# Kernel tuning notes

Measured on AMD Instinct MI355X. Metric: run time of the kernel, lower is better.

The kernel has to match this reference:

```python
import jax, jax.numpy as jnp
import numpy as np

B, NJ, NM = 64, 30, 20
N = NJ * NM          # 600 operation nodes per FJSP instance
IN_DIM, H = 2, 128


def _bn(h):
    # torch BatchNorm1d in training mode, gamma=1/beta=0 (module init), stats over all nodes
    m = h.mean(axis=(0, 1))
    v = h.var(axis=(0, 1))
    return (h - m) / jnp.sqrt(v + 1e-5)


def setup_inputs() -> dict:
    key = jax.random.key(0)
    ks = jax.random.split(key, 20)
    x = jax.random.normal(ks[0], (B, N, IN_DIM), jnp.float32)
    graph_pool = jnp.full((B, N), 1.0 / N, jnp.float32)   # average graph pooling weights
    padded_nei = jnp.zeros((1,), jnp.int32)               # unused (sum pooling path)
    adj = (jax.random.uniform(ks[1], (B, N, N)) < 0.01).astype(jnp.float32)
    adj = jnp.minimum(adj + jnp.eye(N, dtype=jnp.float32)[None], 1.0)  # self-loops
    candidate = jax.random.randint(ks[2], (B, NJ), 0, N)
    a_index = jax.random.randint(ks[3], (B,), 0, NJ)
    mask = jax.random.uniform(ks[4], (B, NJ)) < 0.2
    mask = mask.at[jnp.arange(B), a_index].set(False)     # chosen action never masked
    mask_mch = jax.random.uniform(ks[5], (B, N, NM)) < 0.3
    dur = jax.random.uniform(ks[6], (B, N, NM), dtype=jnp.float32)
    old_action = jax.random.randint(ks[7], (B,), 0, N)
    mch_pool = jax.random.normal(ks[8], (B, H), jnp.float32)

    def w(k, i, o):
        return jax.random.normal(k, (i, o), jnp.float32) * (1.0 / np.sqrt(i))

    z = lambda n: jnp.zeros((n,), jnp.float32)            # biases init to 0 in module
    return dict(
        x=x, graph_pool=graph_pool, padded_nei=padded_nei, adj=adj,
        candidate=candidate, mask=mask, mask_mch=mask_mch, dur=dur,
        a_index=a_index, old_action=old_action, mch_pool=mch_pool,
        W1_0=w(ks[9], IN_DIM, H), b1_0=z(H), W2_0=w(ks[10], H, H), b2_0=z(H),
        W1_1=w(ks[11], H, H), b1_1=z(H), W2_1=w(ks[12], H, H), b2_1=z(H),
        Wa1=w(ks[13], 3 * H, H), ba1=z(H), Wa2=w(ks[14], H, H), ba2=z(H),
        Wa3=w(ks[15], H, 1), ba3=z(1),
        Wc1=w(ks[16], H, H), bc1=z(H), Wc2=w(ks[17], H, 1), bc2=z(1),
    )


def reference(x, graph_pool, padded_nei, adj, candidate, mask, mask_mch, dur,
              a_index, old_action, mch_pool,
              W1_0, b1_0, W2_0, b2_0, W1_1, b1_1, W2_1, b2_1,
              Wa1, ba1, Wa2, ba2, Wa3, ba3, Wc1, bc1, Wc2, bc2):
    # --- GIN encoder: num_layers-1 = 2 message-passing layers, sum pooling ---
    h = x
    for (W1, b1, W2, b2) in ((W1_0, b1_0, W2_0, b2_0), (W1_1, b1_1, W2_1, b2_1)):
        pooled = jnp.einsum('bnm,bmd->bnd', adj, h)         # neighbor sum (adj has self-loops)
        h1 = jax.nn.relu(_bn(pooled @ W1 + b1))             # MLP hidden (BN inside MLP)
        h = jax.nn.relu(_bn(h1 @ W2 + b2))                  # layer BN + relu
    h_nodes = h                                             # [B, N, H]
    h_pooled = jnp.einsum('bn,bnd->bd', graph_pool, h_nodes)  # [B, H]

    # --- gather candidate features, concat pooled contexts ---
    cand_feat = jnp.take_along_axis(h_nodes, candidate[:, :, None], axis=1)  # [B, NJ, H]
    concat = jnp.concatenate([
        cand_feat,
        jnp.broadcast_to(h_pooled[:, None, :], cand_feat.shape),
        jnp.broadcast_to(mch_pool[:, None, :], cand_feat.shape)], axis=-1)   # [B, NJ, 3H]

    # --- MLPActor(3 layers, tanh) ---
    a = jnp.tanh(concat @ Wa1 + ba1)
    a = jnp.tanh(a @ Wa2 + ba2)
    scores = (a @ Wa3 + ba3).squeeze(-1) * 10.0             # [B, NJ]
    scores = jnp.where(mask, -jnp.inf, scores)
    logpi = jax.nn.log_softmax(scores, axis=1)
    pi = jnp.exp(logpi)
    log_a = jnp.take_along_axis(logpi, a_index[:, None], axis=1)[:, 0]
    entropy = -jnp.sum(jnp.where(pi > 0, pi * logpi, 0.0), axis=1)

    # --- gather action-dependent tensors (detached in torch) ---
    b_idx = jnp.arange(B)
    action_node = dur[b_idx, old_action]                    # [B, NM]
    action_feature = h_nodes[b_idx, old_action]             # [B, H]
    mask_mch_action = mask_mch[b_idx, old_action][:, None, :]  # [B, 1, NM]

    # --- MLPCritic(2 layers, tanh) ---
    v = jnp.tanh(h_pooled @ Wc1 + bc1) @ Wc2 + bc2          # [B, 1]

    sg = jax.lax.stop_gradient
    return (entropy, v, log_a, sg(action_node), sg(action_feature),
            mask_mch_action, sg(h_pooled))
```

## Files before the change

### kernel.cpp

```cpp
#include <hip/hip_runtime.h>
#include <hip/hip_bf16.h>

#define BB 64
#define NJ 30
#define NM 20
#define NN 600
#define HH 128
#define NROWS (BB*NN)
#define CAP 48

typedef __attribute__((ext_vector_type(8))) short short8;
typedef __attribute__((ext_vector_type(4))) float f32x4;

#define STATS_B   0
#define FLAGS_B   36864
#define ZERO_B    36880
#define WTB_B     37120
#define NBRCNT_B  143104
#define NBRIDX_B  296704
#define POOLED0_B 7669504
#define T1_B      7976704
#define P1_B      27637504

#define OUT_ENT   0
#define OUT_V     64
#define OUT_LOGA  128
#define OUT_ANODE 192
#define OUT_AFEAT 1472
#define OUT_MMCH  9664
#define OUT_HPOOL 10944

__device__ __forceinline__ bool mask_at(const void* p, int layout, long i) {
    if (layout == 2) return ((const float*)p)[i] != 0.f;
    if (layout == 1) return ((const unsigned char*)p)[i] != 0;
    return ((const int*)p)[i] != 0;
}

__device__ __forceinline__ short bf16rne(float f) {
    unsigned u = __float_as_uint(f);
    return (short)((u + 0x7fffu + ((u >> 16) & 1u)) >> 16);
}
__device__ __forceinline__ float bf2f(unsigned h) {
    return __uint_as_float(h << 16);
}
__device__ __forceinline__ unsigned packbf(float a, float b) {
    return ((unsigned)(unsigned short)bf16rne(a)) |
           (((unsigned)(unsigned short)bf16rne(b)) << 16);
}

__global__ __launch_bounds__(256) void k_sparse(const float* __restrict__ adj,
                                                const float* __restrict__ x,
                                                int* __restrict__ nbr_cnt,
                                                int* __restrict__ nbr_idx,
                                                float* __restrict__ pooled0,
                                                const void* mask_p, const void* maskmch_p,
                                                int* flags,
                                                const float* __restrict__ Wa,
                                                const float* __restrict__ Wb,
                                                const float* __restrict__ Wc,
                                                unsigned short* __restrict__ wT) {
    int bid = blockIdx.x;
    int tid = threadIdx.x;
    if (bid < 289) {
        if (bid >= 97) {
            int bid2 = bid - 97;
            int mat = bid2 >> 6;
            int idx = ((bid2 & 63) << 8) + tid;
            const float* W = mat == 0 ? Wa : (mat == 1 ? Wb : Wc);
            int k = idx >> 7, c = idx & 127;
            wT[mat * 16384 + c * HH + k] = (unsigned short)bf16rne(W[idx]);
        } else {
            unsigned agg = 0;
            int which;
            if (bid == 0) {
                which = 0;
                const unsigned* p = (const unsigned*)mask_p;
                unsigned w0 = (tid < 480) ? p[tid] : 0u;
                unsigned w1 = (tid + 256 < 480) ? p[tid + 256] : 0u;
                agg = w0 | w1;
            } else {
                which = 1;
                const unsigned* p = (const unsigned*)maskmch_p + (size_t)(bid - 1) * 200;
                agg = (tid < 200) ? p[tid] : 0u;
            }
            int f = 0;
            if (((agg >> 24) & 0xffu) == 0x3fu) f |= 1;
            if ((((agg >> 8) & 0xffu) == 1u) || (((agg >> 16) & 0xffu) == 1u) ||
                (((agg >> 24) & 0xffu) == 1u)) f |= 2;
#pragma unroll
            for (int off = 1; off < 64; off <<= 1) f |= __shfl_xor(f, off);
            if ((tid & 63) == 0 && f) atomicOr(&flags[which], f);
        }
    }

    int wrow = bid * 4 + (tid >> 6);
    int lane = tid & 63;
    int b = wrow / NN;
    const float4* arow = (const float4*)(adj + (size_t)wrow * NN);
    int* irow = nbr_idx + (size_t)wrow * CAP;
    const float* xb = x + (size_t)b * NN * 2;
    float4 vv[3];
    vv[0] = arow[lane];
    vv[1] = arow[64 + lane];
    vv[2] = (128 + lane < 150) ? arow[128 + lane] : make_float4(0.f, 0.f, 0.f, 0.f);
    int cnt = 0;
    float p0 = 0.f, p1 = 0.f;
#pragma unroll
    for (int it = 0; it < 3; ++it) {
        float4 v = vv[it];
        int col0 = it * 256 + lane * 4;
        bool m0 = v.x != 0.f, m1 = v.y != 0.f, m2 = v.z != 0.f, m3 = v.w != 0.f;
        int c_lane = (int)m0 + (int)m1 + (int)m2 + (int)m3;
        int inc = c_lane;
#pragma unroll
        for (int off = 1; off < 64; off <<= 1) {
            int t = __shfl_up(inc, off);
            if (lane >= off) inc += t;
        }
        int pos = cnt + inc - c_lane;
        if (m0) {
            if (pos < CAP) irow[pos] = col0;
            float2 xv = *(const float2*)&xb[col0 * 2];
            p0 += xv.x; p1 += xv.y; ++pos;
        }
        if (m1) {
            if (pos < CAP) irow[pos] = col0 + 1;
            float2 xv = *(const float2*)&xb[(col0 + 1) * 2];
            p0 += xv.x; p1 += xv.y; ++pos;
        }
        if (m2) {
            if (pos < CAP) irow[pos] = col0 + 2;
            float2 xv = *(const float2*)&xb[(col0 + 2) * 2];
            p0 += xv.x; p1 += xv.y; ++pos;
        }
        if (m3) {
            if (pos < CAP) irow[pos] = col0 + 3;
            float2 xv = *(const float2*)&xb[(col0 + 3) * 2];
            p0 += xv.x; p1 += xv.y; ++pos;
        }
        cnt += __shfl(inc, 63);
    }
#pragma unroll
    for (int off = 1; off < 64; off <<= 1) {
        p0 += __shfl_xor(p0, off);
        p1 += __shfl_xor(p1, off);
    }
    if (lane == 0) {
        nbr_cnt[wrow] = cnt < CAP ? cnt : CAP;
        pooled0[(size_t)wrow * 2]     = p0;
        pooled0[(size_t)wrow * 2 + 1] = p1;
    }
}

__global__ __launch_bounds__(256) void k_p0stats(const float* __restrict__ pooled0,
                                                 float* __restrict__ out5) {
    __shared__ float red[4][5];
    int i = blockIdx.x * 256 + threadIdx.x;
    float p0 = pooled0[(size_t)i * 2], p1 = pooled0[(size_t)i * 2 + 1];
    float v[5] = {p0, p1, p0 * p0, p1 * p1, p0 * p1};
#pragma unroll
    for (int j = 0; j < 5; ++j)
#pragma unroll
        for (int off = 1; off < 64; off <<= 1) v[j] += __shfl_xor(v[j], off);
    int lane = threadIdx.x & 63, w = threadIdx.x >> 6;
    if (lane == 0)
#pragma unroll
        for (int j = 0; j < 5; ++j) red[w][j] = v[j];
    __syncthreads();
    if (threadIdx.x == 0)
#pragma unroll
        for (int j = 0; j < 5; ++j)
            atomicAdd(&out5[j], red[0][j] + red[1][j] + red[2][j] + red[3][j]);
}

template<int MODE>
__global__ __launch_bounds__(256) void k_stage(const void* __restrict__ t_in_v,
                                               const float* __restrict__ pooled0,
                                               const float* __restrict__ W1,
                                               const unsigned short* __restrict__ wT,
                                               const float* __restrict__ stats_in,
                                               unsigned short* __restrict__ t_out,
                                               float* __restrict__ stats_out) {
    __shared__ float sm_mean[HH], sm_inv[HH];
    __shared__ float smS[4][32], smQ[4][32];
    int tid = threadIdx.x;
    if (MODE == 0 && tid < HH) {
        float S0 = stats_in[0], S1 = stats_in[1], Q0 = stats_in[2], Q1 = stats_in[3], P01 = stats_in[4];
        float w0 = W1[tid], w1 = W1[HH + tid];
        float m = (S0 * w0 + S1 * w1) * (1.f / NROWS);
        float eq = (Q0 * w0 * w0 + Q1 * w1 * w1 + 2.f * P01 * w0 * w1) * (1.f / NROWS);
        sm_mean[tid] = m;
        sm_inv[tid] = 1.f / sqrtf(eq - m * m + 1e-5f);
    }
    if (MODE == 1 && tid < HH) {
        float s = stats_in[tid], q = stats_in[HH + tid];
        float m = s * (1.f / NROWS);
        sm_mean[tid] = m;
        sm_inv[tid] = 1.f / sqrtf(q * (1.f / NROWS) - m * m + 1e-5f);
    }
    __syncthreads();

    const unsigned short* tin = (const unsigned short*)t_in_v;
    int lane = tid & 63, wave = tid >> 6;
    int r16 = lane & 15, kg = lane >> 4;
    int rowbase = (blockIdx.x >> 2) * 64 + wave * 16;
    int colq = blockIdx.x & 3;

    f32x4 acc[2];
#pragma unroll
    for (int t = 0; t < 2; ++t)
#pragma unroll
        for (int i = 0; i < 4; ++i) acc[t][i] = 0.f;

    float p0 = 0.f, p1 = 0.f;
    if (MODE == 0) {
        p0 = pooled0[(size_t)(rowbase + r16) * 2];
        p1 = pooled0[(size_t)(rowbase + r16) * 2 + 1];
    }

#pragma unroll
    for (int ks = 0; ks < 4; ++ks) {
        int kb = ks * 32 + kg * 8;
        short8 afr;
        {
            float av[8];
            if (MODE == 0) {
                float4 wa0 = *(const float4*)&W1[kb];
                float4 wa1 = *(const float4*)&W1[kb + 4];
                float4 wb0 = *(const float4*)&W1[HH + kb];
                float4 wb1 = *(const float4*)&W1[HH + kb + 4];
                av[0] = p0 * wa0.x + p1 * wb0.x; av[1] = p0 * wa0.y + p1 * wb0.y;
                av[2] = p0 * wa0.z + p1 * wb0.z; av[3] = p0 * wa0.w + p1 * wb0.w;
                av[4] = p0 * wa1.x + p1 * wb1.x; av[5] = p0 * wa1.y + p1 * wb1.y;
                av[6] = p0 * wa1.z + p1 * wb1.z; av[7] = p0 * wa1.w + p1 * wb1.w;
            } else {
                short8 raw = *(const short8*)&tin[(size_t)(rowbase + r16) * HH + kb];
#pragma unroll
                for (int j = 0; j < 8; ++j) av[j] = bf2f((unsigned short)raw[j]);
            }
            float4 m0 = *(const float4*)&sm_mean[kb];
            float4 m1 = *(const float4*)&sm_mean[kb + 4];
            float4 i0 = *(const float4*)&sm_inv[kb];
            float4 i1 = *(const float4*)&sm_inv[kb + 4];
            av[0] = fmaxf((av[0] - m0.x) * i0.x, 0.f);
            av[1] = fmaxf((av[1] - m0.y) * i0.y, 0.f);
            av[2] = fmaxf((av[2] - m0.z) * i0.z, 0.f);
            av[3] = fmaxf((av[3] - m0.w) * i0.w, 0.f);
            av[4] = fmaxf((av[4] - m1.x) * i1.x, 0.f);
            av[5] = fmaxf((av[5] - m1.y) * i1.y, 0.f);
            av[6] = fmaxf((av[6] - m1.z) * i1.z, 0.f);
            av[7] = fmaxf((av[7] - m1.w) * i1.w, 0.f);
#pragma unroll
            for (int j = 0; j < 8; ++j) afr[j] = bf16rne(av[j]);
        }
#pragma unroll
        for (int t = 0; t < 2; ++t) {
            short8 bfr = *(const short8*)&wT[(size_t)((colq * 2 + t) * 16 + r16) * HH + kb];
            acc[t] = __builtin_amdgcn_mfma_f32_16x16x32_bf16(afr, bfr, acc[t], 0, 0, 0);
        }
    }

#pragma unroll
    for (int t = 0; t < 2; ++t) {
        int lc = t * 16 + r16;
        int col = colq * 32 + lc;
        float s = 0.f, q = 0.f;
#pragma unroll
        for (int i = 0; i < 4; ++i) {
            float v = acc[t][i];
            t_out[(size_t)(rowbase + kg * 4 + i) * HH + col] = (unsigned short)bf16rne(v);
            s += v; q += v * v;
        }
        s += __shfl_xor(s, 16); q += __shfl_xor(q, 16);
        s += __shfl_xor(s, 32); q += __shfl_xor(q, 32);
        if (kg == 0) { smS[wave][lc] = s; smQ[wave][lc] = q; }
    }
    __syncthreads();
    if (tid < 32) {
        int col = colq * 32 + tid;
        atomicAdd(&stats_out[col],      smS[0][tid] + smS[1][tid] + smS[2][tid] + smS[3][tid]);
        atomicAdd(&stats_out[HH + col], smQ[0][tid] + smQ[1][tid] + smQ[2][tid] + smQ[3][tid]);
    }
}

__global__ __launch_bounds__(256) void k_poolstage(const unsigned short* __restrict__ t1,
                                                   const int* __restrict__ nbr_cnt,
                                                   const int* __restrict__ nbr_idx,
                                                   const float* __restrict__ stats1,
                                                   const unsigned short* __restrict__ wT,
                                                   unsigned short* __restrict__ t_out,
                                                   float* __restrict__ stats_out) {
    __shared__ float sm_mean[HH], sm_inv[HH];
    __shared__ unsigned short shA[32 * HH];
    __shared__ float smS[4][HH], smQ[4][HH];
    int tid = threadIdx.x;
    if (tid < HH) {
        float s = stats1[tid], q = stats1[HH + tid];
        float m = s * (1.f / NROWS);
        sm_mean[tid] = m;
        sm_inv[tid] = 1.f / sqrtf(q * (1.f / NROWS) - m * m + 1e-5f);
    }
    __syncthreads();
    int rowbase = blockIdx.x * 32;

    {
        int r = tid >> 3, cg = tid & 7;
        int row = rowbase + r;
        int b = row / NN;
        int cnt = nbr_cnt[row];
        const int* ir = nbr_idx + (size_t)row * CAP;
        const unsigned short* tb = t1 + (size_t)b * NN * HH + cg * 16;
        float accv[16];
#pragma unroll
        for (int j = 0; j < 16; ++j) accv[j] = 0.f;
        float mloc[16], iloc[16];
#pragma unroll
        for (int j = 0; j < 16; ++j) {
            mloc[j] = sm_mean[cg * 16 + j];
            iloc[j] = sm_inv[cg * 16 + j];
        }
        for (int i = 0; i < cnt; ++i) {
            int m_ = ir[i];
            const unsigned short* p = tb + (size_t)m_ * HH;
            uint2 w0 = *(const uint2*)(p);
            uint2 w1 = *(const uint2*)(p + 4);
            uint2 w2 = *(const uint2*)(p + 8);
            uint2 w3 = *(const uint2*)(p + 12);
            unsigned wsv[8] = {w0.x, w0.y, w1.x, w1.y, w2.x, w2.y, w3.x, w3.y};
#pragma unroll
            for (int j = 0; j < 8; ++j) {
                accv[2 * j]     += fmaxf((bf2f(wsv[j] & 0xffffu) - mloc[2 * j])     * iloc[2 * j], 0.f);
                accv[2 * j + 1] += fmaxf((bf2f(wsv[j] >> 16)     - mloc[2 * j + 1]) * iloc[2 * j + 1], 0.f);
            }
        }
        unsigned short* dst = &shA[r * HH + cg * 16];
#pragma unroll
        for (int j = 0; j < 8; ++j)
            *(unsigned*)(dst + 2 * j) = packbf(accv[2 * j], accv[2 * j + 1]);
    }
    __syncthreads();

    int lane = tid & 63, w = tid >> 6;
    int r16 = lane & 15, kg = lane >> 4;
    int rhalf = w & 1, chalf = w >> 1;
    int rloc = rhalf * 16 + r16;
    short8 afr[4];
#pragma unroll
    for (int ks = 0; ks < 4; ++ks)
        afr[ks] = *(const short8*)&shA[rloc * HH + ks * 32 + kg * 8];
    f32x4 acc[4];
#pragma unroll
    for (int t = 0; t < 4; ++t)
#pragma unroll
        for (int i = 0; i < 4; ++i) acc[t][i] = 0.f;
#pragma unroll
    for (int t = 0; t < 4; ++t) {
        int coltile = chalf * 4 + t;
#pragma unroll
        for (int ks = 0; ks < 4; ++ks) {
            short8 bfr = *(const short8*)&wT[(size_t)(coltile * 16 + r16) * HH + ks * 32 + kg * 8];
            acc[t] = __builtin_amdgcn_mfma_f32_16x16x32_bf16(afr[ks], bfr, acc[t], 0, 0, 0);
        }
    }
#pragma unroll
    for (int t = 0; t < 4; ++t) {
        int col = (chalf * 4 + t) * 16 + r16;
        float s = 0.f, q = 0.f;
#pragma unroll
        for (int i = 0; i < 4; ++i) {
            float v = acc[t][i];
            t_out[(size_t)(rowbase + rhalf * 16 + kg * 4 + i) * HH + col] = (unsigned short)bf16rne(v);
            s += v; q += v * v;
        }
        s += __shfl_xor(s, 16); q += __shfl_xor(q, 16);
        s += __shfl_xor(s, 32); q += __shfl_xor(q, 32);
        if (kg == 0) { smS[w][col] = s; smQ[w][col] = q; }
    }
    __syncthreads();
    if (tid < HH) {
        int col = tid;
        float s, q;
        if (col < 64) { s = smS[0][col] + smS[1][col]; q = smQ[0][col] + smQ[1][col]; }
        else          { s = smS[2][col] + smS[3][col]; q = smQ[2][col] + smQ[3][col]; }
        atomicAdd(&stats_out[col], s);
        atomicAdd(&stats_out[HH + col], q);
    }
}

__global__ __launch_bounds__(256) void k_tail(const unsigned short* __restrict__ t3,
                                              const float* __restrict__ gp,
                                              const float* __restrict__ stats3,
                                              const int* __restrict__ cand,
                                              const float* __restrict__ mch,
                                              const void* __restrict__ mask_p,
                                              const void* __restrict__ maskmch_p,
                                              const int* __restrict__ flags,
                                              const float* __restrict__ dur,
                                              const int* __restrict__ a_index,
                                              const int* __restrict__ old_action,
                                              const float* __restrict__ Wa1,
                                              const float* __restrict__ ba1,
                                              const float* __restrict__ Wa2,
                                              const float* __restrict__ ba2,
                                              const float* __restrict__ Wa3,
                                              const float* __restrict__ ba3,
                                              const float* __restrict__ Wc1,
                                              const float* __restrict__ bc1,
                                              const float* __restrict__ Wc2,
                                              const float* __restrict__ bc2,
                                              float* __restrict__ out) {
    __shared__ float sm_mean[HH], sm_inv[HH], sh_hp[HH], sh_mch[HH], sh_red[HH];
    __shared__ float red8[8][HH];
    __shared__ float sh_cand[NJ][HH];
    __shared__ float sh_a1[NJ][HH];
    __shared__ float sh_sc[NJ][132];
    __shared__ float sh_s[32], sh_lp[32];
    __shared__ int sh_m[32];
    int b = blockIdx.x, tid = threadIdx.x;

    if (tid < HH) {
        float s = stats3[tid], q = stats3[HH + tid];
        float m = s * (1.f / NROWS);
        sm_mean[tid] = m;
        sm_inv[tid] = 1.f / sqrtf(q * (1.f / NROWS) - m * m + 1e-5f);
        sh_mch[tid] = mch[b * HH + tid];
    }
    __syncthreads();

    {
        int c4 = tid & 31, rl = tid >> 5;
        float4 mm = *(const float4*)&sm_mean[c4 * 4];
        float4 iv = *(const float4*)&sm_inv[c4 * 4];
        float a0 = 0.f, a1 = 0.f, a2 = 0.f, a3 = 0.f;
        for (int n = rl; n < NN; n += 8) {
            float w = gp[b * NN + n];
            uint2 t = *(const uint2*)&t3[((size_t)b * NN + n) * HH + c4 * 4];
            a0 += w * fmaxf((bf2f(t.x & 0xffffu) - mm.x) * iv.x, 0.f);
            a1 += w * fmaxf((bf2f(t.x >> 16)     - mm.y) * iv.y, 0.f);
            a2 += w * fmaxf((bf2f(t.y & 0xffffu) - mm.z) * iv.z, 0.f);
            a3 += w * fmaxf((bf2f(t.y >> 16)     - mm.w) * iv.w, 0.f);
        }
        *(float4*)&red8[rl][c4 * 4] = make_float4(a0, a1, a2, a3);
    }
    __syncthreads();
    if (tid < HH) {
        float s = 0.f;
#pragma unroll
        for (int g = 0; g < 8; ++g) s += red8[g][tid];
        sh_hp[tid] = s;
    }
    __syncthreads();

    int c = tid & 127, slot = tid >> 7;
    float mean_c = sm_mean[c], inv_c = sm_inv[c];

    for (int r = slot; r < NJ; r += 2) {
        int cd = cand[b * NJ + r];
        float v = bf2f(t3[((size_t)b * NN + cd) * HH + c]);
        sh_cand[r][c] = fmaxf((v - mean_c) * inv_c, 0.f);
    }
    {
        float part = 0.f;
        const float* src = (slot == 0) ? sh_hp : sh_mch;
        const float* Wp  = Wa1 + (size_t)(slot == 0 ? 128 : 256) * HH;
        for (int k = 0; k < HH; ++k) part += src[k] * Wp[(size_t)k * HH + c];
        red8[slot][c] = part;
    }
    __syncthreads();
    float b2 = red8[0][c] + red8[1][c] + ba1[c];

    for (int r = slot; r < NJ; r += 2) {
        float acc = b2;
        for (int k = 0; k < HH; ++k) acc += sh_cand[r][k] * Wa1[(size_t)k * HH + c];
        sh_a1[r][c] = tanhf(acc);
    }
    __syncthreads();

    {
        float w3 = Wa3[c], bb2 = ba2[c];
        for (int r = slot; r < NJ; r += 2) {
            float acc2 = bb2;
            for (int k = 0; k < HH; ++k) acc2 += sh_a1[r][k] * Wa2[(size_t)k * HH + c];
            sh_sc[r][c] = tanhf(acc2) * w3;
        }
    }
    __syncthreads();
    if (tid < NJ) {
        float s = 0.f;
        for (int c2 = 0; c2 < HH; ++c2) s += sh_sc[tid][c2];
        sh_s[tid] = 10.f * (s + ba3[0]);
    }

    if (tid < HH) {
        float a = bc1[tid];
        for (int k = 0; k < HH; ++k) a += sh_hp[k] * Wc1[(size_t)k * HH + tid];
        sh_red[tid] = tanhf(a) * Wc2[tid];
    }
    __syncthreads();
    for (int st = 64; st > 0; st >>= 1) {
        if (tid < st) sh_red[tid] += sh_red[tid + st];
        __syncthreads();
    }
    if (tid == 0) out[OUT_V + b] = sh_red[0] + bc2[0];

    int fA = flags[0], fB = flags[1];
    int layA = (fA & 1) ? 2 : ((fA & 2) ? 1 : 0);
    int layB = (fB & 1) ? 2 : ((fB & 2) ? 1 : 0);
    if (tid < NJ) sh_m[tid] = mask_at(mask_p, layA, (long)b * NJ + tid) ? 1 : 0;
    __syncthreads();
    if (tid == 0) {
        float mx = -1e30f;
        for (int j = 0; j < NJ; ++j)
            if (!sh_m[j] && sh_s[j] > mx) mx = sh_s[j];
        float sum = 0.f;
        for (int j = 0; j < NJ; ++j)
            if (!sh_m[j]) sum += expf(sh_s[j] - mx);
        float lse = mx + logf(sum);
        float ent = 0.f;
        for (int j = 0; j < NJ; ++j) {
            if (!sh_m[j]) {
                float lp = sh_s[j] - lse;
                sh_lp[j] = lp;
                float pi = expf(lp);
                if (pi > 0.f) ent -= pi * lp;
            }
        }
        out[OUT_ENT + b] = ent;
        out[OUT_LOGA + b] = sh_lp[a_index[b]];
    }

    int old = old_action[b];
    if (tid < NM) {
        out[OUT_ANODE + b * NM + tid] = dur[((size_t)b * NN + old) * NM + tid];
        out[OUT_MMCH + b * NM + tid] =
            mask_at(maskmch_p, layB, ((size_t)b * NN + old) * NM + tid) ? 1.f : 0.f;
    }
    if (tid < HH) {
        float v = bf2f(t3[((size_t)b * NN + old) * HH + tid]);
        out[OUT_AFEAT + b * HH + tid] = fmaxf((v - mean_c) * inv_c, 0.f);
        out[OUT_HPOOL + b * HH + tid] = sh_hp[tid];
    }
}

extern "C" void kernel_launch(void* const* d_in, const int* in_sizes, int n_in,
                              void* d_out, int out_size, void* d_ws, size_t ws_size,
                              hipStream_t stream) {
    (void)in_sizes; (void)n_in; (void)out_size; (void)ws_size;
    const float* x         = (const float*)d_in[0];
    const float* gp        = (const float*)d_in[1];
    const float* adj       = (const float*)d_in[3];
    const int*   cand      = (const int*)d_in[4];
    const void*  mask_p    = d_in[5];
    const void*  maskmch_p = d_in[6];
    const float* dur       = (const float*)d_in[7];
    const int*   a_index   = (const int*)d_in[8];
    const int*   old_act   = (const int*)d_in[9];
    const float* mch_pool  = (const float*)d_in[10];
    const float* W1_0 = (const float*)d_in[11];
    const float* W2_0 = (const float*)d_in[13];
    const float* W1_1 = (const float*)d_in[15];
    const float* W2_1 = (const float*)d_in[17];
    const float* Wa1  = (const float*)d_in[19];
    const float* ba1  = (const float*)d_in[20];
    const float* Wa2  = (const float*)d_in[21];
    const float* ba2  = (const float*)d_in[22];
    const float* Wa3  = (const float*)d_in[23];
    const float* ba3  = (const float*)d_in[24];
    const float* Wc1  = (const float*)d_in[25];
    const float* bc1  = (const float*)d_in[26];
    const float* Wc2  = (const float*)d_in[27];
    const float* bc2  = (const float*)d_in[28];

    char* ws = (char*)d_ws;
    float* stats   = (float*)(ws + STATS_B);
    int*   flags   = (int*)(ws + FLAGS_B);
    unsigned short* wtb = (unsigned short*)(ws + WTB_B);
    int*   nbr_cnt = (int*)(ws + NBRCNT_B);
    int*   nbr_idx = (int*)(ws + NBRIDX_B);
    float* pooled0 = (float*)(ws + POOLED0_B);
    unsigned short* t1_16 = (unsigned short*)(ws + T1_B);
    unsigned short* t2_16 = (unsigned short*)(ws + P1_B);
    float* out     = (float*)d_out;

    hipMemsetAsync(ws, 0, ZERO_B, stream);
    k_sparse<<<NROWS / 4, 256, 0, stream>>>(adj, x, nbr_cnt, nbr_idx, pooled0,
                                            mask_p, maskmch_p, flags, W2_0, W1_1, W2_1, wtb);
    k_p0stats<<<NROWS / 256, 256, 0, stream>>>(pooled0, stats);
    k_stage<0><<<2400, 256, 0, stream>>>(nullptr, pooled0, W1_0, wtb, stats, t1_16, stats + 256);
    k_poolstage<<<NROWS / 32, 256, 0, stream>>>(t1_16, nbr_cnt, nbr_idx, stats + 256,
                                                wtb + 16384, t2_16, stats + 512);
    k_stage<1><<<2400, 256, 0, stream>>>(t2_16, nullptr, nullptr, wtb + 32768, stats + 512,
                                         t1_16, stats + 768);
    k_tail<<<BB, 256, 0, stream>>>(t1_16, gp, stats + 768, cand, mch_pool,
                                   mask_p, maskmch_p, flags, dur, a_index, old_act,
                                   Wa1, ba1, Wa2, ba2, Wa3, ba3, Wc1, bc1, Wc2, bc2, out);
}
```

Baseline: 395.7 us.

## Split tail kernel into pooled-reduction, actor MLP, and final kernels

Replaces the single 64-block tail kernel with three kernels. The graph pooling is split across 8 node chunks per batch and combined with atomics. The actor MLP runs over 240 blocks, each handling 8 candidate rows with register-blocked accumulation over the full 384-wide concat input. A small final kernel then does the softmax, critic and gathers. This spreads the serial tail over more CUs, at the cost of two extra launches and a redundant recompute of the hpool/mch contribution for every candidate row. The hpool buffer sits inside the memset-zeroed region, so the atomics start from zero.

Result: faster. 360.0 us (-9.0%).

```diff
diff --git a/kernel.cpp b/kernel.cpp
--- a/kernel.cpp
+++ b/kernel.cpp
@@ -13,9 +13,11 @@
 typedef __attribute__((ext_vector_type(4))) float f32x4;
 
 #define STATS_B   0
+#define HPOOL_B   4096
 #define FLAGS_B   36864
 #define ZERO_B    36880
 #define WTB_B     37120
+#define SCORES_B  135424
 #define NBRCNT_B  143104
 #define NBRIDX_B  296704
 #define POOLED0_B 7669504
@@ -387,128 +389,162 @@
     }
 }
 
-__global__ __launch_bounds__(256) void k_tail(const unsigned short* __restrict__ t3,
-                                              const float* __restrict__ gp,
-                                              const float* __restrict__ stats3,
-                                              const int* __restrict__ cand,
-                                              const float* __restrict__ mch,
-                                              const void* __restrict__ mask_p,
-                                              const void* __restrict__ maskmch_p,
-                                              const int* __restrict__ flags,
-                                              const float* __restrict__ dur,
-                                              const int* __restrict__ a_index,
-                                              const int* __restrict__ old_action,
-                                              const float* __restrict__ Wa1,
-                                              const float* __restrict__ ba1,
-                                              const float* __restrict__ Wa2,
-                                              const float* __restrict__ ba2,
-                                              const float* __restrict__ Wa3,
-                                              const float* __restrict__ ba3,
-                                              const float* __restrict__ Wc1,
-                                              const float* __restrict__ bc1,
-                                              const float* __restrict__ Wc2,
-                                              const float* __restrict__ bc2,
-                                              float* __restrict__ out) {
-    __shared__ float sm_mean[HH], sm_inv[HH], sh_hp[HH], sh_mch[HH], sh_red[HH];
-    __shared__ float red8[8][HH];
-    __shared__ float sh_cand[NJ][HH];
-    __shared__ float sh_a1[NJ][HH];
-    __shared__ float sh_sc[NJ][132];
-    __shared__ float sh_s[32], sh_lp[32];
-    __shared__ int sh_m[32];
-    int b = blockIdx.x, tid = threadIdx.x;
-
+__global__ __launch_bounds__(256) void k_hpool(const unsigned short* __restrict__ t3,
+                                               const float* __restrict__ gp,
+                                               const float* __restrict__ stats3,
+                                               float* __restrict__ hpool) {
+    __shared__ float sm_mean[HH], sm_inv[HH];
+    __shared__ float red[8][HH];
+    int tid = threadIdx.x;
     if (tid < HH) {
         float s = stats3[tid], q = stats3[HH + tid];
         float m = s * (1.f / NROWS);
         sm_mean[tid] = m;
         sm_inv[tid] = 1.f / sqrtf(q * (1.f / NROWS) - m * m + 1e-5f);
-        sh_mch[tid] = mch[b * HH + tid];
-    }
-    __syncthreads();
-
-    {
-        int c4 = tid & 31, rl = tid >> 5;
-        float4 mm = *(const float4*)&sm_mean[c4 * 4];
-        float4 iv = *(const float4*)&sm_inv[c4 * 4];
-        float a0 = 0.f, a1 = 0.f, a2 = 0.f, a3 = 0.f;
-        for (int n = rl; n < NN; n += 8) {
-            float w = gp[b * NN + n];
-            uint2 t = *(const uint2*)&t3[((size_t)b * NN + n) * HH + c4 * 4];
-            a0 += w * fmaxf((bf2f(t.x & 0xffffu) - mm.x) * iv.x, 0.f);
-            a1 += w * fmaxf((bf2f(t.x >> 16)     - mm.y) * iv.y, 0.f);
-            a2 += w * fmaxf((bf2f(t.y & 0xffffu) - mm.z) * iv.z, 0.f);
-            a3 += w * fmaxf((bf2f(t.y >> 16)     - mm.w) * iv.w, 0.f);
-        }
-        *(float4*)&red8[rl][c4 * 4] = make_float4(a0, a1, a2, a3);
-    }
+    }
+    __syncthreads();
+    int b = blockIdx.x >> 3, chunk = blockIdx.x & 7;
+    int c4 = tid & 31, rl = tid >> 5;
+    float4 mm = *(const float4*)&sm_mean[c4 * 4];
+    float4 iv = *(const float4*)&sm_inv[c4 * 4];
+    float a0 = 0.f, a1 = 0.f, a2 = 0.f, a3 = 0.f;
+    int nend = chunk * 75 + 75;
+    for (int n = chunk * 75 + rl; n < nend; n += 8) {
+        float w = gp[b * NN + n];
+        uint2 t = *(const uint2*)&t3[((size_t)b * NN + n) * HH + c4 * 4];
+        a0 += w * fmaxf((bf2f(t.x & 0xffffu) - mm.x) * iv.x, 0.f);
+        a1 += w * fmaxf((bf2f(t.x >> 16)     - mm.y) * iv.y, 0.f);
+        a2 += w * fmaxf((bf2f(t.y & 0xffffu) - mm.z) * iv.z, 0.f);
+        a3 += w * fmaxf((bf2f(t.y >> 16)     - mm.w) * iv.w, 0.f);
+    }
+    *(float4*)&red[rl][c4 * 4] = make_float4(a0, a1, a2, a3);
     __syncthreads();
     if (tid < HH) {
         float s = 0.f;
 #pragma unroll
-        for (int g = 0; g < 8; ++g) s += red8[g][tid];
-        sh_hp[tid] = s;
-    }
-    __syncthreads();
-
+        for (int g = 0; g < 8; ++g) s += red[g][tid];
+        atomicAdd(&hpool[b * HH + tid], s);
+    }
+}
+
+__global__ __launch_bounds__(256) void k_actor(const unsigned short* __restrict__ t3,
+                                               const int* __restrict__ cand,
+                                               const float* __restrict__ hpool,
+                                               const float* __restrict__ mch,
+                                               const float* __restrict__ stats3,
+                                               const float* __restrict__ Wa1,
+                                               const float* __restrict__ ba1,
+                                               const float* __restrict__ Wa2,
+                                               const float* __restrict__ ba2,
+                                               const float* __restrict__ Wa3,
+                                               const float* __restrict__ ba3,
+                                               float* __restrict__ scores) {
+    __shared__ float sh_c[8 * 384];
+    __shared__ float sh_a1[8 * HH];
+    __shared__ float sred[8][HH];
+    int tid = threadIdx.x;
+    int rbase = blockIdx.x * 8;
     int c = tid & 127, slot = tid >> 7;
-    float mean_c = sm_mean[c], inv_c = sm_inv[c];
-
-    for (int r = slot; r < NJ; r += 2) {
-        int cd = cand[b * NJ + r];
+
+    float mean_c, inv_c;
+    {
+        float s = stats3[c], q = stats3[HH + c];
+        float m = s * (1.f / NROWS);
+        mean_c = m;
+        inv_c = 1.f / sqrtf(q * (1.f / NROWS) - m * m + 1e-5f);
+    }
+#pragma unroll
+    for (int rr = 0; rr < 4; ++rr) {
+        int r = slot * 4 + rr;
+        int row = rbase + r;
+        int b = row / NJ;
+        int cd = cand[row];
         float v = bf2f(t3[((size_t)b * NN + cd) * HH + c]);
-        sh_cand[r][c] = fmaxf((v - mean_c) * inv_c, 0.f);
-    }
+        sh_c[r * 384 + c]       = fmaxf((v - mean_c) * inv_c, 0.f);
+        sh_c[r * 384 + 128 + c] = hpool[b * HH + c];
+        sh_c[r * 384 + 256 + c] = mch[b * HH + c];
+    }
+    __syncthreads();
+
+    float acc[4] = {0.f, 0.f, 0.f, 0.f};
+    for (int k = 0; k < 384; ++k) {
+        float w = Wa1[(size_t)k * HH + c];
+#pragma unroll
+        for (int rr = 0; rr < 4; ++rr)
+            acc[rr] += sh_c[(slot * 4 + rr) * 384 + k] * w;
+    }
+    float bb = ba1[c];
+#pragma unroll
+    for (int rr = 0; rr < 4; ++rr)
+        sh_a1[(slot * 4 + rr) * HH + c] = tanhf(acc[rr] + bb);
+    __syncthreads();
+
+    float acc2[4] = {0.f, 0.f, 0.f, 0.f};
+    for (int k = 0; k < HH; ++k) {
+        float w = Wa2[(size_t)k * HH + c];
+#pragma unroll
+        for (int rr = 0; rr < 4; ++rr)
+            acc2[rr] += sh_a1[(slot * 4 + rr) * HH + k] * w;
+    }
+    float w3 = Wa3[c], bb2 = ba2[c];
+#pragma unroll
+    for (int rr = 0; rr < 4; ++rr)
+        sred[slot * 4 + rr][c] = tanhf(acc2[rr] + bb2) * w3;
+    __syncthreads();
+    int r = tid >> 5, l32 = tid & 31;
+    float v = sred[r][l32] + sred[r][l32 + 32] + sred[r][l32 + 64] + sred[r][l32 + 96];
+    v += __shfl_xor(v, 1); v += __shfl_xor(v, 2); v += __shfl_xor(v, 4);
+    v += __shfl_xor(v, 8); v += __shfl_xor(v, 16);
+    if (l32 == 0) scores[rbase + r] = 10.f * (v + ba3[0]);
+}
+
+__global__ __launch_bounds__(128) void k_final(const unsigned short* __restrict__ t3,
+                                               const float* __restrict__ stats3,
+                                               const float* __restrict__ hpool,
+                                               const float* __restrict__ scores,
+                                               const void* __restrict__ mask_p,
+                                               const void* __restrict__ maskmch_p,
+                                               const int* __restrict__ flags,
+                                               const float* __restrict__ dur,
+                                               const int* __restrict__ a_index,
+                                               const int* __restrict__ old_action,
+                                               const float* __restrict__ Wc1,
+                                               const float* __restrict__ bc1,
+                                               const float* __restrict__ Wc2,
+                                               const float* __restrict__ bc2,
+                                               float* __restrict__ out) {
+    __shared__ float sm_mean[HH], sm_inv[HH], sh_hp[HH], sh_red[HH];
+    __shared__ float sh_s[32], sh_lp[32];
+    __shared__ int sh_m[32];
+    int b = blockIdx.x, t = threadIdx.x;
     {
-        float part = 0.f;
-        const float* src = (slot == 0) ? sh_hp : sh_mch;
-        const float* Wp  = Wa1 + (size_t)(slot == 0 ? 128 : 256) * HH;
-        for (int k = 0; k < HH; ++k) part += src[k] * Wp[(size_t)k * HH + c];
-        red8[slot][c] = part;
-    }
-    __syncthreads();
-    float b2 = red8[0][c] + red8[1][c] + ba1[c];
-
-    for (int r = slot; r < NJ; r += 2) {
-        float acc = b2;
-        for (int k = 0; k < HH; ++k) acc += sh_cand[r][k] * Wa1[(size_t)k * HH + c];
-        sh_a1[r][c] = tanhf(acc);
-    }
-    __syncthreads();
-
-    {
-        float w3 = Wa3[c], bb2 = ba2[c];
-        for (int r = slot; r < NJ; r += 2) {
-            float acc2 = bb2;
-            for (int k = 0; k < HH; ++k) acc2 += sh_a1[r][k] * Wa2[(size_t)k * HH + c];
-            sh_sc[r][c] = tanhf(acc2) * w3;
-        }
-    }
-    __syncthreads();
-    if (tid < NJ) {
-        float s = 0.f;
-        for (int c2 = 0; c2 < HH; ++c2) s += sh_sc[tid][c2];
-        sh_s[tid] = 10.f * (s + ba3[0]);
-    }
-
-    if (tid < HH) {
-        float a = bc1[tid];
-        for (int k = 0; k < HH; ++k) a += sh_hp[k] * Wc1[(size_t)k * HH + tid];
-        sh_red[tid] = tanhf(a) * Wc2[tid];
-    }
+        float s = stats3[t], q = stats3[HH + t];
+        float m = s * (1.f / NROWS);
+        sm_mean[t] = m;
+        sm_inv[t] = 1.f / sqrtf(q * (1.f / NROWS) - m * m + 1e-5f);
+    }
+    sh_hp[t] = hpool[b * HH + t];
+    __syncthreads();
+
+    float acc = bc1[t];
+    for (int k = 0; k < HH; ++k) acc += sh_hp[k] * Wc1[k * HH + t];
+    sh_red[t] = tanhf(acc) * Wc2[t];
     __syncthreads();
     for (int st = 64; st > 0; st >>= 1) {
-        if (tid < st) sh_red[tid] += sh_red[tid + st];
+        if (t < st) sh_red[t] += sh_red[t + st];
         __syncthreads();
     }
-    if (tid == 0) out[OUT_V + b] = sh_red[0] + bc2[0];
+    if (t == 0) out[OUT_V + b] = sh_red[0] + bc2[0];
 
     int fA = flags[0], fB = flags[1];
     int layA = (fA & 1) ? 2 : ((fA & 2) ? 1 : 0);
     int layB = (fB & 1) ? 2 : ((fB & 2) ? 1 : 0);
-    if (tid < NJ) sh_m[tid] = mask_at(mask_p, layA, (long)b * NJ + tid) ? 1 : 0;
-    __syncthreads();
-    if (tid == 0) {
+    if (t < NJ) {
+        sh_s[t] = scores[b * NJ + t];
+        sh_m[t] = mask_at(mask_p, layA, (long)b * NJ + t) ? 1 : 0;
+    }
+    __syncthreads();
+    if (t == 0) {
         float mx = -1e30f;
         for (int j = 0; j < NJ; ++j)
             if (!sh_m[j] && sh_s[j] > mx) mx = sh_s[j];
@@ -530,15 +566,15 @@
     }
 
     int old = old_action[b];
-    if (tid < NM) {
-        out[OUT_ANODE + b * NM + tid] = dur[((size_t)b * NN + old) * NM + tid];
-        out[OUT_MMCH + b * NM + tid] =
-            mask_at(maskmch_p, layB, ((size_t)b * NN + old) * NM + tid) ? 1.f : 0.f;
-    }
-    if (tid < HH) {
-        float v = bf2f(t3[((size_t)b * NN + old) * HH + tid]);
-        out[OUT_AFEAT + b * HH + tid] = fmaxf((v - mean_c) * inv_c, 0.f);
-        out[OUT_HPOOL + b * HH + tid] = sh_hp[tid];
+    if (t < NM) {
+        out[OUT_ANODE + b * NM + t] = dur[((size_t)b * NN + old) * NM + t];
+        out[OUT_MMCH + b * NM + t] =
+            mask_at(maskmch_p, layB, ((size_t)b * NN + old) * NM + t) ? 1.f : 0.f;
+    }
+    {
+        float v = bf2f(t3[((size_t)b * NN + old) * HH + t]);
+        out[OUT_AFEAT + b * HH + t] = fmaxf((v - sm_mean[t]) * sm_inv[t], 0.f);
+        out[OUT_HPOOL + b * HH + t] = sh_hp[t];
     }
 }
 
@@ -573,8 +609,10 @@
 
     char* ws = (char*)d_ws;
     float* stats   = (float*)(ws + STATS_B);
+    float* hpool   = (float*)(ws + HPOOL_B);
     int*   flags   = (int*)(ws + FLAGS_B);
     unsigned short* wtb = (unsigned short*)(ws + WTB_B);
+    float* scores  = (float*)(ws + SCORES_B);
     int*   nbr_cnt = (int*)(ws + NBRCNT_B);
     int*   nbr_idx = (int*)(ws + NBRIDX_B);
     float* pooled0 = (float*)(ws + POOLED0_B);
@@ -591,7 +629,9 @@
                                                 wtb + 16384, t2_16, stats + 512);
     k_stage<1><<<2400, 256, 0, stream>>>(t2_16, nullptr, nullptr, wtb + 32768, stats + 512,
                                          t1_16, stats + 768);
-    k_tail<<<BB, 256, 0, stream>>>(t1_16, gp, stats + 768, cand, mch_pool,
-                                   mask_p, maskmch_p, flags, dur, a_index, old_act,
-                                   Wa1, ba1, Wa2, ba2, Wa3, ba3, Wc1, bc1, Wc2, bc2, out);
-}
+    k_hpool<<<BB * 8, 256, 0, stream>>>(t1_16, gp, stats + 768, hpool);
+    k_actor<<<240, 256, 0, stream>>>(t1_16, cand, hpool, mch_pool, stats + 768,
+                                     Wa1, ba1, Wa2, ba2, Wa3, ba3, scores);
+    k_final<<<BB, 128, 0, stream>>>(t1_16, stats + 768, hpool, scores, mask_p, maskmch_p, flags,
+                                    dur, a_index, old_act, Wc1, bc1, Wc2, bc2, out);
+}
```
